# Kernel optimization log

Hardware: AMD Instinct MI355X
Metric: run time of the kernel (lower is better)

## Reference

```python
import jax, jax.numpy as jnp
import numpy as np

N = 262144  # number of points / sequence length
D = 64      # feature dim (qkv_dim); deterministic features => nb_features == D
KERNEL_EPSILON = 1e-3


def setup_inputs() -> dict:
    key = jax.random.key(0)
    ks = jax.random.split(key, 7)
    s = 1.0 / np.sqrt(D)
    return {
        "x": jax.random.normal(ks[0], (N, D), dtype=jnp.float32),
        "Wq": jax.random.normal(ks[1], (D, D), dtype=jnp.float32) * s,
        "bq": jnp.zeros((D,), dtype=jnp.float32),
        "Wk": jax.random.normal(ks[2], (D, D), dtype=jnp.float32) * s,
        "bk": jnp.zeros((D,), dtype=jnp.float32),
        "Wv": jax.random.normal(ks[3], (D, D), dtype=jnp.float32) * s,
        "bv": jnp.zeros((D,), dtype=jnp.float32),
    }


def reference(x, Wq, bq, Wk, bk, Wv, bv):
    # Dense projections (flax nn.Dense: x @ W + b)
    q = x @ Wq + bq  # [N, D]
    k = x @ Wk + bk
    v = x @ Wv + bv
    # Deterministic generalized kernel feature map: relu(data) + kernel_epsilon
    qp = jax.nn.relu(q) + KERNEL_EPSILON  # [N, M], M == D
    kp = jax.nn.relu(k) + KERNEL_EPSILON  # [N, M]
    # Bidirectional FAVOR+ linear attention: O(N*M*D)
    kv = jnp.einsum("nm,nd->md", kp, v)       # [M, D]
    num = jnp.einsum("nm,md->nd", qp, kv)     # [N, D]
    # renormalize_attention=True: divide by qp . sum(kp)
    denom = qp @ kp.sum(axis=0)               # [N]
    return num / denom[:, None]
```

## Files before the change

### kernel.cpp

```cpp
#include <hip/hip_runtime.h>
#include <hip/hip_bf16.h>


#define NPTS 262144
#define TILES (NPTS / 64)
#define GRID1 512
#define TPB1 (TILES / GRID1)
#define GRID2 512
#define TPB2 (TILES / GRID2)
#define L2STRIDE 4112
#define EPS 1e-3f

typedef __attribute__((ext_vector_type(8))) short short8;
typedef __attribute__((ext_vector_type(4))) float f32x4;

__device__ __forceinline__ unsigned short f2bf(float f) {
    unsigned u = __builtin_bit_cast(unsigned, f);
    u += 0x7FFFu + ((u >> 16) & 1u);
    return (unsigned short)(u >> 16);
}

__device__ __forceinline__ short8 cvt8(float4 p0, float4 p1) {
    short8 a;
    a[0] = (short)f2bf(p0.x); a[1] = (short)f2bf(p0.y); a[2] = (short)f2bf(p0.z); a[3] = (short)f2bf(p0.w);
    a[4] = (short)f2bf(p1.x); a[5] = (short)f2bf(p1.y); a[6] = (short)f2bf(p1.z); a[7] = (short)f2bf(p1.w);
    return a;
}

__device__ __forceinline__ void lds_barrier() {
    asm volatile("s_waitcnt lgkmcnt(0)" ::: "memory");
    __builtin_amdgcn_s_barrier();
}

__device__ __forceinline__ void stage_mat(const float* __restrict__ W,
                                          unsigned short (*dst)[72], int srow, int sc0) {
    const float* p = W + srow * 64 + sc0;
    float4 f0 = ((const float4*)p)[0];
    float4 f1 = ((const float4*)p)[1];
    float4 f2 = ((const float4*)p)[2];
    float4 f3 = ((const float4*)p)[3];
    float ff[16] = {f0.x, f0.y, f0.z, f0.w, f1.x, f1.y, f1.z, f1.w,
                    f2.x, f2.y, f2.z, f2.w, f3.x, f3.y, f3.z, f3.w};
    unsigned hh[8];
#pragma unroll
    for (int e = 0; e < 8; ++e)
        hh[e] = (unsigned)f2bf(ff[2 * e]) | ((unsigned)f2bf(ff[2 * e + 1]) << 16);
    uint4 u0 = {hh[0], hh[1], hh[2], hh[3]};
    uint4 u1 = {hh[4], hh[5], hh[6], hh[7]};
    *(uint4*)&dst[srow][sc0] = u0;
    *(uint4*)&dst[srow][sc0 + 8] = u1;
}

__global__ __launch_bounds__(256, 4) void pass1_kernel(
    const float* __restrict__ x,
    const float* __restrict__ Wk, const float* __restrict__ bk,
    const float* __restrict__ Wv, const float* __restrict__ bv,
    float* __restrict__ kvPart, float* __restrict__ ksPart)
{
    __shared__ unsigned short kpT[64][72];
    __shared__ unsigned short vT[64][72];
    __shared__ unsigned short wkF[8][64][8];
    __shared__ unsigned short wvF[8][64][8];

    const int tid = threadIdx.x;
    const int w = tid >> 6, l = tid & 63, l15 = l & 15, lg = l >> 4;
    const int srow = tid >> 2, sc0 = (tid & 3) * 16;

    {
        const float* Ws[2] = {Wk, Wv};
        unsigned short (*Fs[2])[64][8] = {wkF, wvF};
#pragma unroll
        for (int m = 0; m < 2; ++m) {
            stage_mat(Ws[m], kpT, srow, sc0);
            __syncthreads();
#pragma unroll
            for (int kk = 0; kk < 2; ++kk) {
                short8 t;
#pragma unroll
                for (int e = 0; e < 8; ++e)
                    t[e] = (short)kpT[kk * 32 + lg * 8 + e][w * 16 + l15];
                *(short8*)&Fs[m][w * 2 + kk][l][0] = t;
            }
            __syncthreads();
        }
    }
    float bkl[4], bvl[4];
#pragma unroll
    for (int j = 0; j < 4; ++j) { bkl[j] = bk[j * 16 + l15]; bvl[j] = bv[j * 16 + l15]; }

    f32x4 akv[4];
#pragma unroll
    for (int j = 0; j < 4; ++j) akv[j] = (f32x4){0.f, 0.f, 0.f, 0.f};
    float ks[4] = {0.f, 0.f, 0.f, 0.f};

    const int t0 = blockIdx.x * TPB1;
    const float* xbase = x + ((size_t)t0 * 64 + w * 16 + l15) * 64 + lg * 8;
    float4 c0 = *(const float4*)(xbase + 0);
    float4 c1 = *(const float4*)(xbase + 4);
    float4 c2 = *(const float4*)(xbase + 32);
    float4 c3 = *(const float4*)(xbase + 36);
    const int nbase = w * 16 + lg * 4;

    for (int t = 0; t < TPB1; ++t) {
        const float* xn = xbase + (size_t)((t + 1 < TPB1) ? (t + 1) : t) * 4096;
        float4 n0 = *(const float4*)(xn + 0);
        float4 n1 = *(const float4*)(xn + 4);
        float4 n2 = *(const float4*)(xn + 32);
        float4 n3 = *(const float4*)(xn + 36);

        short8 a0 = cvt8(c0, c1);
        short8 a1 = cvt8(c2, c3);

#pragma unroll
        for (int j = 0; j < 4; ++j) {
            short8 bk0 = *(const short8*)&wkF[j * 2 + 0][l][0];
            short8 bk1 = *(const short8*)&wkF[j * 2 + 1][l][0];
            short8 bv0 = *(const short8*)&wvF[j * 2 + 0][l][0];
            short8 bv1 = *(const short8*)&wvF[j * 2 + 1][l][0];
            f32x4 z = (f32x4){0.f, 0.f, 0.f, 0.f};
            f32x4 ak = __builtin_amdgcn_mfma_f32_16x16x32_bf16(a0, bk0, z, 0, 0, 0);
            ak = __builtin_amdgcn_mfma_f32_16x16x32_bf16(a1, bk1, ak, 0, 0, 0);
            f32x4 av = __builtin_amdgcn_mfma_f32_16x16x32_bf16(a0, bv0, z, 0, 0, 0);
            av = __builtin_amdgcn_mfma_f32_16x16x32_bf16(a1, bv1, av, 0, 0, 0);
            unsigned short h[4], g[4];
#pragma unroll
            for (int r = 0; r < 4; ++r) {
                float kp = fmaxf(ak[r] + bkl[j], 0.f) + EPS;
                ks[j] += kp;
                h[r] = f2bf(kp);
                g[r] = f2bf(av[r] + bvl[j]);
            }
            uint2 hp = {(unsigned)h[0] | ((unsigned)h[1] << 16), (unsigned)h[2] | ((unsigned)h[3] << 16)};
            uint2 gp = {(unsigned)g[0] | ((unsigned)g[1] << 16), (unsigned)g[2] | ((unsigned)g[3] << 16)};
            *(uint2*)&kpT[j * 16 + l15][nbase] = hp;
            *(uint2*)&vT[j * 16 + l15][nbase] = gp;
        }
        lds_barrier();
        short8 ka0 = *(const short8*)&kpT[w * 16 + l15][lg * 8];
        short8 ka1 = *(const short8*)&kpT[w * 16 + l15][32 + lg * 8];
#pragma unroll
        for (int j = 0; j < 4; ++j) {
            short8 vb0 = *(const short8*)&vT[j * 16 + l15][lg * 8];
            short8 vb1 = *(const short8*)&vT[j * 16 + l15][32 + lg * 8];
            akv[j] = __builtin_amdgcn_mfma_f32_16x16x32_bf16(ka0, vb0, akv[j], 0, 0, 0);
            akv[j] = __builtin_amdgcn_mfma_f32_16x16x32_bf16(ka1, vb1, akv[j], 0, 0, 0);
        }
        lds_barrier();
        c0 = n0; c1 = n1; c2 = n2; c3 = n3;
    }

    float* kvs = kvPart + (size_t)blockIdx.x * 4096;
#pragma unroll
    for (int j = 0; j < 4; ++j)
#pragma unroll
        for (int r = 0; r < 4; ++r)
            kvs[(size_t)(w * 16 + lg * 4 + r) * 64 + j * 16 + l15] = akv[j][r];
#pragma unroll
    for (int j = 0; j < 4; ++j) {
        float s = ks[j];
        s += __shfl_xor(s, 16, 64);
        s += __shfl_xor(s, 32, 64);
        if (lg == 0) ksPart[(size_t)blockIdx.x * 256 + w * 64 + j * 16 + l15] = s;
    }
}

__global__ __launch_bounds__(256, 4) void reduceA_kernel(
    const float* __restrict__ kvPart, const float* __restrict__ ksPart,
    float* __restrict__ l2kv, float* __restrict__ l2ks)
{
    const int b = blockIdx.x, t = threadIdx.x;
    if (b < 128) {
        f32x4 acc[4];
#pragma unroll
        for (int si = 0; si < 4; ++si) acc[si] = (f32x4){0.f, 0.f, 0.f, 0.f};
        const float* base = kvPart + (size_t)b * 4 * 4096;
#pragma unroll
        for (int r = 0; r < 4; ++r)
#pragma unroll
            for (int si = 0; si < 4; ++si)
                acc[si] += *(const f32x4*)(base + (size_t)r * 4096 + si * 1024 + t * 4);
#pragma unroll
        for (int si = 0; si < 4; ++si)
            *(f32x4*)(l2kv + (size_t)b * L2STRIDE + si * 1024 + t * 4) = acc[si];
    } else {
        const int i = b - 128;
        float acc = 0.f;
        const float* p = ksPart + (size_t)i * 128 * 256 + t;
#pragma unroll 8
        for (int r = 0; r < 128; ++r) acc += p[(size_t)r * 256];
        l2ks[i * 256 + t] = acc;
    }
}

__global__ __launch_bounds__(256, 4) void reduceB_kernel(
    const float* __restrict__ l2kv, const float* __restrict__ l2ks,
    float* __restrict__ kvFin, float* __restrict__ ksFin)
{
    const int b = blockIdx.x, t = threadIdx.x;
    if (b < 4) {
        f32x4 acc = (f32x4){0.f, 0.f, 0.f, 0.f};
        const float* p = l2kv + b * 1024 + t * 4;
#pragma unroll 8
        for (int s = 0; s < 128; ++s) acc += *(const f32x4*)(p + (size_t)s * L2STRIDE);
        *(f32x4*)(kvFin + b * 1024 + t * 4) = acc;
    } else if (t < 64) {
        float s = 0.f;
#pragma unroll
        for (int i = 0; i < 16; ++i) s += l2ks[i * 64 + t];
        ksFin[t] = s;
    }
}

__global__ __launch_bounds__(256, 2) void pass2_kernel(
    const float* __restrict__ x, const float* __restrict__ Wq, const float* __restrict__ bq,
    const float* __restrict__ kvFin, const float* __restrict__ ksFin,
    float* __restrict__ out)
{
    __shared__ unsigned short stageS[64][72];
    __shared__ unsigned short wqF[8][64][8];

    const int tid = threadIdx.x;
    const int w = tid >> 6, l = tid & 63, l15 = l & 15, lg = l >> 4;
    const int srow = tid >> 2, sc0 = (tid & 3) * 16;

    stage_mat(Wq, stageS, srow, sc0);
    __syncthreads();
    {
#pragma unroll
        for (int kk = 0; kk < 2; ++kk) {
            short8 t;
#pragma unroll
            for (int e = 0; e < 8; ++e)
                t[e] = (short)stageS[kk * 32 + lg * 8 + e][w * 16 + l15];
            *(short8*)&wqF[w * 2 + kk][l][0] = t;
        }
    }
    __syncthreads();
    stage_mat(kvFin, stageS, srow, sc0);
    __syncthreads();
    short8 kvA[4][2];
#pragma unroll
    for (int dj = 0; dj < 4; ++dj)
#pragma unroll
        for (int kk = 0; kk < 2; ++kk) {
            short8 t;
#pragma unroll
            for (int e = 0; e < 8; ++e) {
                int m = (kk * 2 + (e >> 2)) * 16 + lg * 4 + (e & 3);
                t[e] = (short)stageS[m][dj * 16 + l15];
            }
            kvA[dj][kk] = t;
        }
    float bql2[4][4], ksl2[4][4];
#pragma unroll
    for (int jm = 0; jm < 4; ++jm)
#pragma unroll
        for (int r = 0; r < 4; ++r) {
            bql2[jm][r] = bq[jm * 16 + lg * 4 + r];
            ksl2[jm][r] = ksFin[jm * 16 + lg * 4 + r];
        }

    const int t0 = blockIdx.x * TPB2;
    const float* xbase = x + ((size_t)t0 * 64 + w * 16 + l15) * 64 + lg * 8;
    float4 c0 = *(const float4*)(xbase + 0);
    float4 c1 = *(const float4*)(xbase + 4);
    float4 c2 = *(const float4*)(xbase + 32);
    float4 c3 = *(const float4*)(xbase + 36);

    for (int t = 0; t < TPB2; ++t) {
        const float* xn = xbase + (size_t)((t + 1 < TPB2) ? (t + 1) : t) * 4096;
        float4 n0 = *(const float4*)(xn + 0);
        float4 n1 = *(const float4*)(xn + 4);
        float4 n2 = *(const float4*)(xn + 32);
        float4 n3 = *(const float4*)(xn + 36);

        short8 a0 = cvt8(c0, c1);
        short8 a1 = cvt8(c2, c3);

        const f32x4 z = (f32x4){0.f, 0.f, 0.f, 0.f};
        float dp = 0.f;
        short8 qb0, qb1;
#pragma unroll
        for (int jm = 0; jm < 4; ++jm) {
            short8 wq0 = *(const short8*)&wqF[jm * 2 + 0][l][0];
            short8 wq1 = *(const short8*)&wqF[jm * 2 + 1][l][0];
            f32x4 aq = __builtin_amdgcn_mfma_f32_16x16x32_bf16(wq0, a0, z, 0, 0, 0);
            aq = __builtin_amdgcn_mfma_f32_16x16x32_bf16(wq1, a1, aq, 0, 0, 0);
#pragma unroll
            for (int r = 0; r < 4; ++r) {
                float qv = fmaxf(aq[r] + bql2[jm][r], 0.f) + EPS;
                dp += qv * ksl2[jm][r];
                unsigned short h = f2bf(qv);
                if (jm < 2) qb0[(jm & 1) * 4 + r] = (short)h;
                else        qb1[(jm & 1) * 4 + r] = (short)h;
            }
        }
        dp += __shfl_xor(dp, 16, 64);
        dp += __shfl_xor(dp, 32, 64);
        const float inv = __builtin_amdgcn_rcpf(dp);

        const size_t nrow = (size_t)(t0 + t) * 64 + w * 16 + l15;
#pragma unroll
        for (int dj = 0; dj < 4; ++dj) {
            f32x4 nm = __builtin_amdgcn_mfma_f32_16x16x32_bf16(kvA[dj][0], qb0, z, 0, 0, 0);
            nm = __builtin_amdgcn_mfma_f32_16x16x32_bf16(kvA[dj][1], qb1, nm, 0, 0, 0);
            f32x4 o4 = {nm[0] * inv, nm[1] * inv, nm[2] * inv, nm[3] * inv};
            *(f32x4*)(out + nrow * 64 + dj * 16 + lg * 4) = o4;
        }
        c0 = n0; c1 = n1; c2 = n2; c3 = n3;
    }
}

extern "C" void kernel_launch(void* const* d_in, const int* in_sizes, int n_in,
                              void* d_out, int out_size, void* d_ws, size_t ws_size,
                              hipStream_t stream)
{
    const float* x  = (const float*)d_in[0];
    const float* Wq = (const float*)d_in[1];
    const float* bq = (const float*)d_in[2];
    const float* Wk = (const float*)d_in[3];
    const float* bk = (const float*)d_in[4];
    const float* Wv = (const float*)d_in[5];
    const float* bv = (const float*)d_in[6];
    float* out = (float*)d_out;

    float* kvPart = (float*)d_ws;
    float* ksPart = kvPart + (size_t)GRID1 * 4096;
    float* l2kv   = ksPart + (size_t)GRID1 * 256;
    float* l2ks   = l2kv + (size_t)128 * L2STRIDE;
    float* kvFin  = l2ks + 4 * 256;
    float* ksFin  = kvFin + 4096;

    hipLaunchKernelGGL(pass1_kernel, dim3(GRID1), dim3(256), 0, stream,
                       x, Wk, bk, Wv, bv, kvPart, ksPart);
    hipLaunchKernelGGL(reduceA_kernel, dim3(132), dim3(256), 0, stream,
                       kvPart, ksPart, l2kv, l2ks);
    hipLaunchKernelGGL(reduceB_kernel, dim3(5), dim3(256), 0, stream,
                       l2kv, l2ks, kvFin, ksFin);
    hipLaunchKernelGGL(pass2_kernel, dim3(GRID2), dim3(256), 0, stream,
                       x, Wq, bq, kvFin, ksFin, out);
}
```

Measured before the change: 60.31 us.

## Merge two-stage partial reduction into one kernel using float atomics

Replaces the two-level reduction (reduceA into an L2 buffer, then reduceB) with a single reduce kernel of 20 blocks that each sum 32 partials and atomically add into the final kv/ks buffers. The final buffers are zeroed by block 0 of pass1, which removes one kernel launch and the intermediate buffer round trip. In exchange, each of the 16 kv blocks reads 32 partials serially with fewer blocks in flight, there is atomic contention on the 4096-float output, and the summation order becomes nondeterministic.

Result: faster. 54.33 us (-9.9%).

```diff
diff --git a/kernel.cpp b/kernel.cpp
--- a/kernel.cpp
+++ b/kernel.cpp
@@ -8,7 +8,6 @@
 #define TPB1 (TILES / GRID1)
 #define GRID2 512
 #define TPB2 (TILES / GRID2)
-#define L2STRIDE 4112
 #define EPS 1e-3f
 
 typedef __attribute__((ext_vector_type(8))) short short8;
@@ -55,7 +54,8 @@
     const float* __restrict__ x,
     const float* __restrict__ Wk, const float* __restrict__ bk,
     const float* __restrict__ Wv, const float* __restrict__ bv,
-    float* __restrict__ kvPart, float* __restrict__ ksPart)
+    float* __restrict__ kvPart, float* __restrict__ ksPart,
+    float* __restrict__ kvFin, float* __restrict__ ksFin)
 {
     __shared__ unsigned short kpT[64][72];
     __shared__ unsigned short vT[64][72];
@@ -65,6 +65,14 @@
     const int tid = threadIdx.x;
     const int w = tid >> 6, l = tid & 63, l15 = l & 15, lg = l >> 4;
     const int srow = tid >> 2, sc0 = (tid & 3) * 16;
+
+    if (blockIdx.x == 0) {
+        const f32x4 z4 = (f32x4){0.f, 0.f, 0.f, 0.f};
+#pragma unroll
+        for (int i = 0; i < 4; ++i)
+            *(f32x4*)(kvFin + tid * 16 + i * 4) = z4;
+        if (tid < 64) ksFin[tid] = 0.f;
+    }
 
     {
         const float* Ws[2] = {Wk, Wv};
@@ -164,50 +172,33 @@
     }
 }
 
-__global__ __launch_bounds__(256, 4) void reduceA_kernel(
+__global__ __launch_bounds__(256, 4) void reduce_kernel(
     const float* __restrict__ kvPart, const float* __restrict__ ksPart,
-    float* __restrict__ l2kv, float* __restrict__ l2ks)
+    float* __restrict__ kvFin, float* __restrict__ ksFin)
 {
     const int b = blockIdx.x, t = threadIdx.x;
-    if (b < 128) {
+    if (b < 16) {
         f32x4 acc[4];
 #pragma unroll
         for (int si = 0; si < 4; ++si) acc[si] = (f32x4){0.f, 0.f, 0.f, 0.f};
-        const float* base = kvPart + (size_t)b * 4 * 4096;
-#pragma unroll
-        for (int r = 0; r < 4; ++r)
+        const float* base = kvPart + (size_t)b * 32 * 4096;
+#pragma unroll 4
+        for (int r = 0; r < 32; ++r)
 #pragma unroll
             for (int si = 0; si < 4; ++si)
                 acc[si] += *(const f32x4*)(base + (size_t)r * 4096 + si * 1024 + t * 4);
 #pragma unroll
         for (int si = 0; si < 4; ++si)
-            *(f32x4*)(l2kv + (size_t)b * L2STRIDE + si * 1024 + t * 4) = acc[si];
+#pragma unroll
+            for (int e = 0; e < 4; ++e)
+                unsafeAtomicAdd(&kvFin[si * 1024 + t * 4 + e], acc[si][e]);
     } else {
-        const int i = b - 128;
+        const int i = b - 16;
         float acc = 0.f;
         const float* p = ksPart + (size_t)i * 128 * 256 + t;
 #pragma unroll 8
         for (int r = 0; r < 128; ++r) acc += p[(size_t)r * 256];
-        l2ks[i * 256 + t] = acc;
-    }
-}
-
-__global__ __launch_bounds__(256, 4) void reduceB_kernel(
-    const float* __restrict__ l2kv, const float* __restrict__ l2ks,
-    float* __restrict__ kvFin, float* __restrict__ ksFin)
-{
-    const int b = blockIdx.x, t = threadIdx.x;
-    if (b < 4) {
-        f32x4 acc = (f32x4){0.f, 0.f, 0.f, 0.f};
-        const float* p = l2kv + b * 1024 + t * 4;
-#pragma unroll 8
-        for (int s = 0; s < 128; ++s) acc += *(const f32x4*)(p + (size_t)s * L2STRIDE);
-        *(f32x4*)(kvFin + b * 1024 + t * 4) = acc;
-    } else if (t < 64) {
-        float s = 0.f;
-#pragma unroll
-        for (int i = 0; i < 16; ++i) s += l2ks[i * 64 + t];
-        ksFin[t] = s;
+        unsafeAtomicAdd(&ksFin[t & 63], acc);
     }
 }
 
@@ -326,17 +317,13 @@
 
     float* kvPart = (float*)d_ws;
     float* ksPart = kvPart + (size_t)GRID1 * 4096;
-    float* l2kv   = ksPart + (size_t)GRID1 * 256;
-    float* l2ks   = l2kv + (size_t)128 * L2STRIDE;
-    float* kvFin  = l2ks + 4 * 256;
+    float* kvFin  = ksPart + (size_t)GRID1 * 256;
     float* ksFin  = kvFin + 4096;
 
     hipLaunchKernelGGL(pass1_kernel, dim3(GRID1), dim3(256), 0, stream,
-                       x, Wk, bk, Wv, bv, kvPart, ksPart);
-    hipLaunchKernelGGL(reduceA_kernel, dim3(132), dim3(256), 0, stream,
-                       kvPart, ksPart, l2kv, l2ks);
-    hipLaunchKernelGGL(reduceB_kernel, dim3(5), dim3(256), 0, stream,
-                       l2kv, l2ks, kvFin, ksFin);
+                       x, Wk, bk, Wv, bv, kvPart, ksPart, kvFin, ksFin);
+    hipLaunchKernelGGL(reduce_kernel, dim3(20), dim3(256), 0, stream,
+                       kvPart, ksPart, kvFin, ksFin);
     hipLaunchKernelGGL(pass2_kernel, dim3(GRID2), dim3(256), 0, stream,
                        x, Wq, bq, kvFin, ksFin, out);
 }
```
